# Kernel tuning notes

Hardware: AMD Instinct MI355X
Metric: run time of the kernel (lower is better)

## Reference

```python
import jax, jax.numpy as jnp
import numpy as np

B, S, D, H, E, TOP_K = 4, 2048, 1024, 2048, 8, 2


def setup_inputs() -> dict:
    key = jax.random.key(0)
    ks = jax.random.split(key, 5)
    scale_d = 1.0 / np.sqrt(D)
    scale_h = 1.0 / np.sqrt(H)
    return {
        "x": jax.random.normal(ks[0], (B, S, D), dtype=jnp.float32),
        "gate_w": jax.random.normal(ks[1], (D, E), dtype=jnp.float32) * scale_d,
        "w1": jax.random.normal(ks[2], (E, D, H), dtype=jnp.float32) * scale_d,
        "w2": jax.random.normal(ks[3], (E, D, H), dtype=jnp.float32) * scale_d,
        "w3": jax.random.normal(ks[4], (E, H, D), dtype=jnp.float32) * scale_h,
    }


def reference(x, gate_w, w1, w2, w3):
    # Gating: softmax over experts, keep top-k probs, renormalize.
    gate_scores = jax.nn.softmax(x @ gate_w, axis=-1)          # [B,S,E]
    top_vals, top_idx = jax.lax.top_k(gate_scores, TOP_K)      # [B,S,K]
    mask = (jax.nn.one_hot(top_idx, E, dtype=x.dtype) * top_vals[..., None]).sum(axis=-2)  # [B,S,E]
    weights = mask / (mask.sum(axis=-1, keepdims=True) + 1e-9)
    # Dense SwiGLU over ALL experts (faithful to the original ModuleList loop).
    g = jax.nn.silu(jnp.einsum('bsd,edh->bseh', x, w1)) * jnp.einsum('bsd,edh->bseh', x, w2)  # [B,S,E,H]
    expert_out = jnp.einsum('bseh,ehd->bsed', g, w3)           # [B,S,E,D]
    # Masked weighted combine (dropout is identity in eval / p=0).
    return jnp.einsum('bse,bsed->bsd', weights, expert_out)    # [B,S,D]
```

## Files before the change

kernel.cpp:

```cpp
#include <hip/hip_runtime.h>

#define T_TOK 8192
#define DDIM 1024
#define HDIM 2048
#define NEXP 8

typedef __attribute__((ext_vector_type(8))) short short8;
typedef __attribute__((ext_vector_type(4))) float f32x4;

#define WAITV8 asm volatile("s_waitcnt vmcnt(8)" ::: "memory")
#define WAITV0 asm volatile("s_waitcnt vmcnt(0)" ::: "memory")
#define WAITL0 asm volatile("s_waitcnt lgkmcnt(0)" ::: "memory")
#define SCHEDB __builtin_amdgcn_sched_barrier(0)
#define BARRIER __builtin_amdgcn_s_barrier()

__device__ __forceinline__ unsigned short f2bf(float f) {
  unsigned int u = __builtin_bit_cast(unsigned int, f);
  u += 0x7fffu + ((u >> 16) & 1u);
  return (unsigned short)(u >> 16);
}
__device__ __forceinline__ float bf2f(unsigned short h) {
  unsigned int u = ((unsigned int)h) << 16;
  return __builtin_bit_cast(float, u);
}
__device__ __forceinline__ void gload16(const void* g, void* l) {
  __builtin_amdgcn_global_load_lds((const __attribute__((address_space(1))) void*)g,
                                   (__attribute__((address_space(3))) void*)l, 16, 0, 0);
}
__device__ __forceinline__ int imin(int a, int b) { return a < b ? a : b; }

__global__ __launch_bounds__(256) void cvt_kernel(const float* __restrict__ in,
                                                  unsigned short* __restrict__ out, int n) {
  int i = (blockIdx.x * 256 + threadIdx.x) * 8;
  int stride = gridDim.x * 256 * 8;
  for (; i < n; i += stride) {
    float4 a = *(const float4*)(in + i);
    float4 b = *(const float4*)(in + i + 4);
    alignas(16) unsigned short t[8] = {f2bf(a.x), f2bf(a.y), f2bf(a.z), f2bf(a.w),
                                       f2bf(b.x), f2bf(b.y), f2bf(b.z), f2bf(b.w)};
    *(uint4*)(out + i) = *(const uint4*)t;
  }
}

__global__ __launch_bounds__(256) void tcvt_kernel(const float* __restrict__ in,
                                                   unsigned short* __restrict__ out,
                                                   int R, int C, size_t outEstride,
                                                   int perm, int s16) {
  int e = blockIdx.z;
  int rb = blockIdx.y * 64, cb = blockIdx.x * 64;
  const float* inE = in + (size_t)e * R * C;
  unsigned short* outE = out + (size_t)e * outEstride;
  __shared__ float tile[64][65];
  int tid = threadIdx.x;
  #pragma unroll
  for (int i = 0; i < 4; ++i) {
    int f = tid + i * 256;
    int r = f >> 4, c4 = (f & 15) << 2;
    float4 v = *(const float4*)(inE + (size_t)(rb + r) * C + cb + c4);
    tile[r][c4] = v.x; tile[r][c4 + 1] = v.y; tile[r][c4 + 2] = v.z; tile[r][c4 + 3] = v.w;
  }
  __syncthreads();
  #pragma unroll
  for (int i = 0; i < 2; ++i) {
    int g = tid + i * 256;
    int oc = g >> 3;
    int r8 = (g & 7) << 3;
    alignas(16) unsigned short tmp[8];
    #pragma unroll
    for (int j = 0; j < 8; ++j) tmp[j] = f2bf(tile[r8 + j][oc]);
    int orow = cb + oc;
    int orow2 = perm ? (32 * (orow >> 4) + (orow & 15) + s16) : orow;
    *(uint4*)(outE + (size_t)orow2 * R + rb + r8) = *(const uint4*)tmp;
  }
}

__global__ __launch_bounds__(256) void gate_kernel(const float* __restrict__ x,
                                                   const float* __restrict__ gw,
                                                   int* __restrict__ t_exp,
                                                   float* __restrict__ t_w) {
  int t = blockIdx.x * 4 + (threadIdx.x >> 6);
  int lane = threadIdx.x & 63;
  const float* xp = x + (size_t)t * DDIM;
  float acc[NEXP];
  #pragma unroll
  for (int e = 0; e < NEXP; ++e) acc[e] = 0.f;
  for (int i = 0; i < DDIM / 64; ++i) {
    int d = i * 64 + lane;
    float xv = xp[d];
    const float* g = gw + d * NEXP;
    #pragma unroll
    for (int e = 0; e < NEXP; ++e) acc[e] += xv * g[e];
  }
  #pragma unroll
  for (int off = 32; off > 0; off >>= 1) {
    #pragma unroll
    for (int e = 0; e < NEXP; ++e) acc[e] += __shfl_xor(acc[e], off, 64);
  }
  float mx = acc[0];
  #pragma unroll
  for (int e = 1; e < NEXP; ++e) mx = fmaxf(mx, acc[e]);
  float p[NEXP]; float S = 0.f;
  #pragma unroll
  for (int e = 0; e < NEXP; ++e) { p[e] = expf(acc[e] - mx); S += p[e]; }
  int i0 = 0; float v0 = p[0];
  #pragma unroll
  for (int e = 1; e < NEXP; ++e) if (p[e] > v0) { v0 = p[e]; i0 = e; }
  int i1 = -1; float v1 = -1.f;
  #pragma unroll
  for (int e = 0; e < NEXP; ++e) if (e != i0 && p[e] > v1) { v1 = p[e]; i1 = e; }
  float pv0 = v0 / S, pv1 = v1 / S;
  float denom = pv0 + pv1 + 1e-9f;
  if (lane == 0) {
    t_exp[t * 2] = i0; t_exp[t * 2 + 1] = i1;
    t_w[t * 2] = pv0 / denom; t_w[t * 2 + 1] = pv1 / denom;
  }
}

__global__ __launch_bounds__(1024) void partition_kernel(
    const int* __restrict__ t_exp, const float* __restrict__ t_w,
    int* __restrict__ ctrl, int* __restrict__ row_tok,
    float* __restrict__ row_w, int* __restrict__ inv_row) {
  int tid = threadIdx.x;
  int wv = tid >> 6, lane = tid & 63;
  __shared__ int wtot[16][8];
  __shared__ int wbase[16][8];
  __shared__ int soff[8];

  int t0 = tid * 8;
  int exps[16];
  int c[8];
  #pragma unroll
  for (int e = 0; e < 8; ++e) c[e] = 0;
  #pragma unroll
  for (int s = 0; s < 16; ++s) {
    exps[s] = t_exp[t0 * 2 + s];
    #pragma unroll
    for (int e = 0; e < 8; ++e) c[e] += (exps[s] == e);
  }
  int inc[8];
  #pragma unroll
  for (int e = 0; e < 8; ++e) inc[e] = c[e];
  #pragma unroll
  for (int d = 1; d < 64; d <<= 1) {
    #pragma unroll
    for (int e = 0; e < 8; ++e) {
      int v = __shfl_up(inc[e], d, 64);
      if (lane >= d) inc[e] += v;
    }
  }
  if (lane == 63) {
    #pragma unroll
    for (int e = 0; e < 8; ++e) wtot[wv][e] = inc[e];
  }
  __syncthreads();
  if (wv == 0 && lane < 16) {
    #pragma unroll
    for (int e = 0; e < 8; ++e) {
      int b = 0;
      for (int w = 0; w < 16; ++w)
        if (w < lane) b += wtot[w][e];
      wbase[lane][e] = b;
    }
  }
  __syncthreads();
  if (tid == 0) {
    int o = 0;
    #pragma unroll
    for (int e = 0; e < 8; ++e) {
      int tot = wbase[15][e] + wtot[15][e];
      ctrl[e] = tot; ctrl[8 + e] = o; soff[e] = o; o += tot;
    }
  }
  __syncthreads();
  int base[8];
  #pragma unroll
  for (int e = 0; e < 8; ++e) base[e] = soff[e] + wbase[wv][e] + (inc[e] - c[e]);
  #pragma unroll
  for (int s = 0; s < 16; ++s) {
    int ee = exps[s];
    float w = t_w[t0 * 2 + s];
    int pos = 0;
    #pragma unroll
    for (int e = 0; e < 8; ++e)
      if (ee == e) { pos = base[e]; base[e] = base[e] + 1; }
    row_tok[pos] = t0 + (s >> 1);
    row_w[pos] = w;
    inv_row[t0 * 2 + s] = pos;
  }
}


#define PHASE(BUF, MH_, STG) do {                                          \
    short8 av[4];                                                          \
    if (MH_ == 0) {                                                        \
      _Pragma("unroll")                                                    \
      for (int n = 0; n < 4; ++n)                                          \
        bv[n] = *(const short8*)(&lds[BUF][1][0] + bOff + n * 512);        \
    }                                                                      \
    _Pragma("unroll")                                                      \
    for (int m = 0; m < 4; ++m)                                            \
      av[m] = *(const short8*)(&lds[BUF][0][0] + aOff + (MH_ * 4 + m) * 512); \
    STG;                                                                   \
    WAITV8;                                                                \
    BARRIER;                                                               \
    WAITL0; SCHEDB;                                                        \
    __builtin_amdgcn_s_setprio(1);                                         \
    _Pragma("unroll")                                                      \
    for (int m = 0; m < 4; ++m)                                            \
      _Pragma("unroll")                                                    \
      for (int n = 0; n < 4; ++n)                                          \
        acc[MH_ * 4 + m][n] = __builtin_amdgcn_mfma_f32_16x16x32_bf16(av[m], bv[n], acc[MH_ * 4 + m][n], 0, 0, 0); \
    __builtin_amdgcn_s_setprio(0);                                         \
    BARRIER;                                                               \
} while (0)

#define STA(SB, KO) do {                                                   \
    gload16(aQ0 + (KO), &lds[SB][0][0] + tid * 8);                         \
    gload16(aQ1 + (KO), &lds[SB][0][0] + 4096 + tid * 8); } while (0)
#define STB(SB, KO) do {                                                   \
    gload16(bQ0 + (KO), &lds[SB][1][0] + tid * 8);                         \
    gload16(bQ1 + (KO), &lds[SB][1][0] + 4096 + tid * 8); } while (0)

#define K_PIPELINE(NT)                                                     \
  WAITV0;                                                                  \
  STA(0, 0);  STB(0, 0);                                                   \
  STA(1, 32); STB(1, 32);                                                  \
  STA(2, 64); STB(2, 64);                                                  \
  WAITV8; BARRIER;                                                         \
  _Pragma("unroll 1")                                                      \
  for (int t = 0; t < (NT); ++t) {                                         \
    int buf = t & 3;                                                       \
    int tc = imin(t + 3, (NT) - 1);                                        \
    int sb = tc & 3;                                                       \
    int ko = tc * 32;                                                      \
    PHASE(buf, 0, STA(sb, ko));                                            \
    PHASE(buf, 1, STB(sb, ko));                                            \
  }

__global__ __launch_bounds__(512, 1) void gemm1_kernel(
    const unsigned short* __restrict__ xbf,
    const unsigned short* __restrict__ w12t,
    const int* __restrict__ row_tok, const float* __restrict__ row_w,
    const int* __restrict__ ctrl, unsigned short* __restrict__ G) {
  int bid = blockIdx.x;
  int e = bid & 7;
  int j = bid >> 3;
  int nt = ((j >> 5) << 2) | (j & 3);
  int mt0 = (j >> 2) & 7;
  int cnt = ctrl[e];
  if (mt0 * 256 >= cnt) return;
  int off = ctrl[8 + e];

  __shared__ unsigned short lds[4][2][8192];

  int tid = threadIdx.x, lane = tid & 63;
  const unsigned short* w12e = w12t + (size_t)e * (4096 * 1024);

  int sr = tid >> 2;
  int cS8 = ((tid & 3) ^ (sr & 3) ^ ((sr >> 2) & 3)) * 8;
  const unsigned short* bQ0 = w12e + (size_t)(nt * 256 + sr) * 1024 + cS8;
  const unsigned short* bQ1 = w12e + (size_t)(nt * 256 + 128 + sr) * 1024 + cS8;

  int wid = tid >> 6, wr = wid >> 2, wc = wid & 3;
  int lr16 = lane & 15, hi = lane >> 4;
  int klane = (lr16 & 3) ^ ((lr16 >> 2) & 3);
  int aOff = (wr * 128 + lr16) * 32 + ((hi ^ klane) * 8);
  int bOff = (wc * 64 + lr16) * 32 + ((hi ^ klane) * 8);

  #pragma unroll 1
  for (int mt = mt0; mt * 256 < cnt; mt += 8) {
    int tokA = row_tok[off + imin(mt * 256 + sr, cnt - 1)];
    int tokB = row_tok[off + imin(mt * 256 + 128 + sr, cnt - 1)];
    const unsigned short* aQ0 = xbf + (size_t)tokA * 1024 + cS8;
    const unsigned short* aQ1 = xbf + (size_t)tokB * 1024 + cS8;

    f32x4 z = {0.f, 0.f, 0.f, 0.f};
    f32x4 acc[8][4];
    #pragma unroll
    for (int m = 0; m < 8; ++m)
      #pragma unroll
      for (int n = 0; n < 4; ++n) acc[m][n] = z;
    short8 bv[4];

    K_PIPELINE(32)

    #pragma unroll
    for (int m = 0; m < 8; ++m)
      #pragma unroll
      for (int jj = 0; jj < 4; ++jj) {
        int rl = mt * 256 + wr * 128 + (m >> 2) * 64 + (m & 3) * 16 + hi * 4 + jj;
        if (rl < cnt) {
          float wrj = row_w[off + rl];
          size_t base = (size_t)(off + rl) * HDIM + nt * 128 + wc * 32 + lr16;
          float h1 = acc[m][0][jj], h2 = acc[m][1][jj];
          G[base] = f2bf((h1 / (1.f + __expf(-h1))) * h2 * wrj);
          h1 = acc[m][2][jj]; h2 = acc[m][3][jj];
          G[base + 16] = f2bf((h1 / (1.f + __expf(-h1))) * h2 * wrj);
        }
      }
  }
}

__global__ __launch_bounds__(512, 1) void gemm2_kernel(
    const unsigned short* __restrict__ G,
    const unsigned short* __restrict__ w3t,
    const int* __restrict__ ctrl, unsigned short* __restrict__ Y) {
  int bid = blockIdx.x;
  int e = bid & 7;
  int j = bid >> 3;
  int nt = j >> 3;
  int mt0 = j & 7;
  int cnt = ctrl[e];
  if (mt0 * 256 >= cnt) return;
  int off = ctrl[8 + e];

  __shared__ unsigned short lds[4][2][8192];

  int tid = threadIdx.x, lane = tid & 63;
  const unsigned short* w3e = w3t + (size_t)e * (1024 * 2048);

  int sr = tid >> 2;
  int cS8 = ((tid & 3) ^ (sr & 3) ^ ((sr >> 2) & 3)) * 8;
  const unsigned short* bQ0 = w3e + (size_t)(nt * 256 + sr) * 2048 + cS8;
  const unsigned short* bQ1 = w3e + (size_t)(nt * 256 + 128 + sr) * 2048 + cS8;

  int wid = tid >> 6, wr = wid >> 2, wc = wid & 3;
  int lr16 = lane & 15, hi = lane >> 4;
  int klane = (lr16 & 3) ^ ((lr16 >> 2) & 3);
  int aOff = (wr * 128 + lr16) * 32 + ((hi ^ klane) * 8);
  int bOff = (wc * 64 + lr16) * 32 + ((hi ^ klane) * 8);

  #pragma unroll 1
  for (int mt = mt0; mt * 256 < cnt; mt += 8) {
    const unsigned short* aQ0 =
        G + (size_t)(off + imin(mt * 256 + sr, cnt - 1)) * 2048 + cS8;
    const unsigned short* aQ1 =
        G + (size_t)(off + imin(mt * 256 + 128 + sr, cnt - 1)) * 2048 + cS8;

    f32x4 z = {0.f, 0.f, 0.f, 0.f};
    f32x4 acc[8][4];
    #pragma unroll
    for (int m = 0; m < 8; ++m)
      #pragma unroll
      for (int n = 0; n < 4; ++n) acc[m][n] = z;
    short8 bv[4];

    K_PIPELINE(64)

    #pragma unroll
    for (int m = 0; m < 8; ++m)
      #pragma unroll
      for (int jj = 0; jj < 4; ++jj) {
        int rl = mt * 256 + wr * 128 + (m >> 2) * 64 + (m & 3) * 16 + hi * 4 + jj;
        if (rl < cnt) {
          size_t yrow = (size_t)(off + rl) * DDIM + nt * 256 + wc * 64 + lr16;
          #pragma unroll
          for (int n = 0; n < 4; ++n) Y[yrow + n * 16] = f2bf(acc[m][n][jj]);
        }
      }
  }
}

__global__ __launch_bounds__(256) void combine_kernel(const unsigned short* __restrict__ Y,
                                                      const int* __restrict__ inv_row,
                                                      float* __restrict__ out) {
  int gid = blockIdx.x * 256 + threadIdx.x;
  int t = gid >> 7;
  int cidx = (gid & 127) * 8;
  int rA = inv_row[t * 2], rB = inv_row[t * 2 + 1];
  uint4 va = *(const uint4*)(Y + (size_t)rA * DDIM + cidx);
  uint4 vb = *(const uint4*)(Y + (size_t)rB * DDIM + cidx);
  const unsigned short* pa = (const unsigned short*)&va;
  const unsigned short* pb = (const unsigned short*)&vb;
  float4 o0, o1;
  o0.x = bf2f(pa[0]) + bf2f(pb[0]); o0.y = bf2f(pa[1]) + bf2f(pb[1]);
  o0.z = bf2f(pa[2]) + bf2f(pb[2]); o0.w = bf2f(pa[3]) + bf2f(pb[3]);
  o1.x = bf2f(pa[4]) + bf2f(pb[4]); o1.y = bf2f(pa[5]) + bf2f(pb[5]);
  o1.z = bf2f(pa[6]) + bf2f(pb[6]); o1.w = bf2f(pa[7]) + bf2f(pb[7]);
  float* op = out + (size_t)t * DDIM + cidx;
  *(float4*)op = o0;
  *(float4*)(op + 4) = o1;
}

extern "C" void kernel_launch(void* const* d_in, const int* in_sizes, int n_in,
                              void* d_out, int out_size, void* d_ws, size_t ws_size,
                              hipStream_t stream) {
  const float* x  = (const float*)d_in[0];
  const float* gw = (const float*)d_in[1];
  const float* w1 = (const float*)d_in[2];
  const float* w2 = (const float*)d_in[3];
  const float* w3 = (const float*)d_in[4];
  float* out = (float*)d_out;
  char* ws = (char*)d_ws;

  unsigned short* xbf  = (unsigned short*)(ws + 0);
  unsigned short* w12t = (unsigned short*)(ws + 16777216);
  unsigned short* w3t  = (unsigned short*)(ws + 83886080);
  unsigned short* G    = (unsigned short*)(ws + 117440512);
  unsigned short* Y    = (unsigned short*)(ws + 184549376);
  int*   row_tok = (int*)  (ws + 218103808);
  float* row_w   = (float*)(ws + 218169344);
  int*   inv_row = (int*)  (ws + 218234880);
  int*   t_exp   = (int*)  (ws + 218300416);
  float* t_w     = (float*)(ws + 218365952);
  int*   ctrl    = (int*)  (ws + 218431488);

  cvt_kernel<<<4096, 256, 0, stream>>>(x, xbf, T_TOK * DDIM);
  tcvt_kernel<<<dim3(32, 16, 8), 256, 0, stream>>>(w1, w12t, 1024, 2048,
                                                   (size_t)4096 * 1024, 1, 0);
  tcvt_kernel<<<dim3(32, 16, 8), 256, 0, stream>>>(w2, w12t, 1024, 2048,
                                                   (size_t)4096 * 1024, 1, 16);
  tcvt_kernel<<<dim3(16, 32, 8), 256, 0, stream>>>(w3, w3t, 2048, 1024,
                                                   (size_t)1024 * 2048, 0, 0);

  gate_kernel<<<2048, 256, 0, stream>>>(x, gw, t_exp, t_w);
  partition_kernel<<<1, 1024, 0, stream>>>(t_exp, t_w, ctrl, row_tok, row_w, inv_row);

  gemm1_kernel<<<1024, 512, 0, stream>>>(xbf, w12t, row_tok, row_w, ctrl, G);
  gemm2_kernel<<<256, 512, 0, stream>>>(G, w3t, ctrl, Y);
  combine_kernel<<<4096, 256, 0, stream>>>(Y, inv_row, out);
}
```

Before: 421.6 us.

## Collapse two-phase K loop into single barrier step and simplify LDS swizzle

Replaces the two half-phases per K tile, each with two barriers and separately staged A and B loads, with one step per K tile. Each step issues all four global-to-LDS loads for the tile three ahead, waits on one barrier, then reads all A and B fragments and runs all 32 MFMAs. The LDS XOR swizzle changes to a simpler (row>>1)&3 pattern, and the epilogue row mapping is updated to match. The aim is to halve barrier and wait overhead per K tile, at the cost of more live fragment registers and possible changes in LDS bank conflicts or in MFMA/load overlap.

```diff
diff --git a/kernel.cpp b/kernel.cpp
--- a/kernel.cpp
+++ b/kernel.cpp
@@ -190,52 +190,34 @@
 }
 
 
-#define PHASE(BUF, MH_, STG) do {                                          \
-    short8 av[4];                                                          \
-    if (MH_ == 0) {                                                        \
+#define KSTEP(T_, NT_) do {                                                \
+    int buf_ = (T_) & 3;                                                   \
+    WAITV8;                                                                \
+    BARRIER;                                                               \
+    int tc_ = imin((T_) + 3, (NT_) - 1);                                   \
+    STG(tc_ & 3, tc_);                                                     \
+    short8 av[8], bv[4];                                                   \
+    _Pragma("unroll")                                                      \
+    for (int n = 0; n < 4; ++n)                                            \
+      bv[n] = *(const short8*)(&lds[buf_][1][0] + bOff + n * 512);         \
+    _Pragma("unroll")                                                      \
+    for (int m = 0; m < 8; ++m)                                            \
+      av[m] = *(const short8*)(&lds[buf_][0][0] + aOff + m * 512);         \
+    __builtin_amdgcn_s_setprio(1);                                         \
+    _Pragma("unroll")                                                      \
+    for (int m = 0; m < 8; ++m)                                            \
       _Pragma("unroll")                                                    \
       for (int n = 0; n < 4; ++n)                                          \
-        bv[n] = *(const short8*)(&lds[BUF][1][0] + bOff + n * 512);        \
-    }                                                                      \
-    _Pragma("unroll")                                                      \
-    for (int m = 0; m < 4; ++m)                                            \
-      av[m] = *(const short8*)(&lds[BUF][0][0] + aOff + (MH_ * 4 + m) * 512); \
-    STG;                                                                   \
-    WAITV8;                                                                \
-    BARRIER;                                                               \
-    WAITL0; SCHEDB;                                                        \
-    __builtin_amdgcn_s_setprio(1);                                         \
-    _Pragma("unroll")                                                      \
-    for (int m = 0; m < 4; ++m)                                            \
-      _Pragma("unroll")                                                    \
-      for (int n = 0; n < 4; ++n)                                          \
-        acc[MH_ * 4 + m][n] = __builtin_amdgcn_mfma_f32_16x16x32_bf16(av[m], bv[n], acc[MH_ * 4 + m][n], 0, 0, 0); \
+        acc[m][n] = __builtin_amdgcn_mfma_f32_16x16x32_bf16(av[m], bv[n], acc[m][n], 0, 0, 0); \
     __builtin_amdgcn_s_setprio(0);                                         \
-    BARRIER;                                                               \
+    WAITL0;                                                                \
 } while (0)
 
-#define STA(SB, KO) do {                                                   \
-    gload16(aQ0 + (KO), &lds[SB][0][0] + tid * 8);                         \
-    gload16(aQ1 + (KO), &lds[SB][0][0] + 4096 + tid * 8); } while (0)
-#define STB(SB, KO) do {                                                   \
-    gload16(bQ0 + (KO), &lds[SB][1][0] + tid * 8);                         \
-    gload16(bQ1 + (KO), &lds[SB][1][0] + 4096 + tid * 8); } while (0)
-
-#define K_PIPELINE(NT)                                                     \
+#define K_PIPELINE(NT_)                                                    \
   WAITV0;                                                                  \
-  STA(0, 0);  STB(0, 0);                                                   \
-  STA(1, 32); STB(1, 32);                                                  \
-  STA(2, 64); STB(2, 64);                                                  \
-  WAITV8; BARRIER;                                                         \
+  STG(0, 0); STG(1, 1); STG(2, 2);                                         \
   _Pragma("unroll 1")                                                      \
-  for (int t = 0; t < (NT); ++t) {                                         \
-    int buf = t & 3;                                                       \
-    int tc = imin(t + 3, (NT) - 1);                                        \
-    int sb = tc & 3;                                                       \
-    int ko = tc * 32;                                                      \
-    PHASE(buf, 0, STA(sb, ko));                                            \
-    PHASE(buf, 1, STB(sb, ko));                                            \
-  }
+  for (int t = 0; t < (NT_); ++t) { KSTEP(t, (NT_)); }
 
 __global__ __launch_bounds__(512, 1) void gemm1_kernel(
     const unsigned short* __restrict__ xbf,
@@ -257,15 +239,21 @@
   const unsigned short* w12e = w12t + (size_t)e * (4096 * 1024);
 
   int sr = tid >> 2;
-  int cS8 = ((tid & 3) ^ (sr & 3) ^ ((sr >> 2) & 3)) * 8;
+  int cS8 = ((tid & 3) ^ ((sr >> 1) & 3)) * 8;
   const unsigned short* bQ0 = w12e + (size_t)(nt * 256 + sr) * 1024 + cS8;
   const unsigned short* bQ1 = w12e + (size_t)(nt * 256 + 128 + sr) * 1024 + cS8;
 
   int wid = tid >> 6, wr = wid >> 2, wc = wid & 3;
   int lr16 = lane & 15, hi = lane >> 4;
-  int klane = (lr16 & 3) ^ ((lr16 >> 2) & 3);
-  int aOff = (wr * 128 + lr16) * 32 + ((hi ^ klane) * 8);
-  int bOff = (wc * 64 + lr16) * 32 + ((hi ^ klane) * 8);
+  int koff = (hi ^ ((lr16 >> 1) & 3)) * 8;
+  int aOff = (wr * 128 + lr16) * 32 + koff;
+  int bOff = (wc * 64 + lr16) * 32 + koff;
+
+#define STG(SB, T_) do {                                                   \
+    gload16(aQ0 + (T_) * 32, &lds[SB][0][0] + tid * 8);                    \
+    gload16(aQ1 + (T_) * 32, &lds[SB][0][0] + 4096 + tid * 8);             \
+    gload16(bQ0 + (T_) * 32, &lds[SB][1][0] + tid * 8);                    \
+    gload16(bQ1 + (T_) * 32, &lds[SB][1][0] + 4096 + tid * 8); } while (0)
 
   #pragma unroll 1
   for (int mt = mt0; mt * 256 < cnt; mt += 8) {
@@ -280,7 +268,6 @@
     for (int m = 0; m < 8; ++m)
       #pragma unroll
       for (int n = 0; n < 4; ++n) acc[m][n] = z;
-    short8 bv[4];
 
     K_PIPELINE(32)
 
@@ -288,7 +275,7 @@
     for (int m = 0; m < 8; ++m)
       #pragma unroll
       for (int jj = 0; jj < 4; ++jj) {
-        int rl = mt * 256 + wr * 128 + (m >> 2) * 64 + (m & 3) * 16 + hi * 4 + jj;
+        int rl = mt * 256 + wr * 128 + m * 16 + hi * 4 + jj;
         if (rl < cnt) {
           float wrj = row_w[off + rl];
           size_t base = (size_t)(off + rl) * HDIM + nt * 128 + wc * 32 + lr16;
@@ -299,6 +286,7 @@
         }
       }
   }
+#undef STG
 }
 
 __global__ __launch_bounds__(512, 1) void gemm2_kernel(
@@ -320,15 +308,21 @@
   const unsigned short* w3e = w3t + (size_t)e * (1024 * 2048);
 
   int sr = tid >> 2;
-  int cS8 = ((tid & 3) ^ (sr & 3) ^ ((sr >> 2) & 3)) * 8;
+  int cS8 = ((tid & 3) ^ ((sr >> 1) & 3)) * 8;
   const unsigned short* bQ0 = w3e + (size_t)(nt * 256 + sr) * 2048 + cS8;
   const unsigned short* bQ1 = w3e + (size_t)(nt * 256 + 128 + sr) * 2048 + cS8;
 
   int wid = tid >> 6, wr = wid >> 2, wc = wid & 3;
   int lr16 = lane & 15, hi = lane >> 4;
-  int klane = (lr16 & 3) ^ ((lr16 >> 2) & 3);
-  int aOff = (wr * 128 + lr16) * 32 + ((hi ^ klane) * 8);
-  int bOff = (wc * 64 + lr16) * 32 + ((hi ^ klane) * 8);
+  int koff = (hi ^ ((lr16 >> 1) & 3)) * 8;
+  int aOff = (wr * 128 + lr16) * 32 + koff;
+  int bOff = (wc * 64 + lr16) * 32 + koff;
+
+#define STG(SB, T_) do {                                                   \
+    gload16(aQ0 + (T_) * 32, &lds[SB][0][0] + tid * 8);                    \
+    gload16(aQ1 + (T_) * 32, &lds[SB][0][0] + 4096 + tid * 8);             \
+    gload16(bQ0 + (T_) * 32, &lds[SB][1][0] + tid * 8);                    \
+    gload16(bQ1 + (T_) * 32, &lds[SB][1][0] + 4096 + tid * 8); } while (0)
 
   #pragma unroll 1
   for (int mt = mt0; mt * 256 < cnt; mt += 8) {
@@ -343,7 +337,6 @@
     for (int m = 0; m < 8; ++m)
       #pragma unroll
       for (int n = 0; n < 4; ++n) acc[m][n] = z;
-    short8 bv[4];
 
     K_PIPELINE(64)
 
@@ -351,7 +344,7 @@
     for (int m = 0; m < 8; ++m)
       #pragma unroll
       for (int jj = 0; jj < 4; ++jj) {
-        int rl = mt * 256 + wr * 128 + (m >> 2) * 64 + (m & 3) * 16 + hi * 4 + jj;
+        int rl = mt * 256 + wr * 128 + m * 16 + hi * 4 + jj;
         if (rl < cnt) {
           size_t yrow = (size_t)(off + rl) * DDIM + nt * 256 + wc * 64 + lr16;
           #pragma unroll
@@ -359,6 +352,7 @@
         }
       }
   }
+#undef STG
 }
 
 __global__ __launch_bounds__(256) void combine_kernel(const unsigned short* __restrict__ Y,
```

Result: faster. 400.2 us (-5.1%).
